# Performance work log

Measured on AMD Instinct MI355X. Metric: run time of the kernel, lower is better.

The kernel has to match this reference:

```python
import jax, jax.numpy as jnp
import numpy as np

EPS = 1e-6
MAX_ACOSH_ARG = 1e6
MAX_DIST = 50.0
TINY = 1e-15
B, T, D = 2, 512, 512
H, N = 8, 32
A = N + 1
TAU = 1.0


def mink(x, y):
    # Lorentzian inner product over last (ambient) dim
    return -x[..., 0] * y[..., 0] + jnp.sum(x[..., 1:] * y[..., 1:], axis=-1)


def project_to_hyperboloid(x):
    xx = mink(x, x)
    scale = jnp.sqrt(jnp.maximum(jnp.abs(xx), TINY))[..., None]
    x = x / scale
    return jnp.concatenate([jnp.abs(x[..., :1]), x[..., 1:]], axis=-1)


def exp_map(p, v):
    vn = jnp.sqrt(jnp.maximum(mink(v, v), TINY))[..., None]
    y = jnp.cosh(vn) * p + (jnp.sinh(vn) / jnp.maximum(vn, TINY)) * v
    return project_to_hyperboloid(y)


def log_map(p, y):
    alpha = jnp.clip(-mink(p, y), 1.0 + EPS, MAX_ACOSH_ARG)
    dist = jnp.arccosh(alpha)[..., None]
    u = y + alpha[..., None] * p
    un = jnp.sqrt(jnp.maximum(mink(u, u), TINY))[..., None]
    return dist / jnp.maximum(un, TINY) * u


def _lift(x, W, b):
    # Linear lift -> (B,H,T,N), append time-like 0, expmap at origin
    u = (jnp.einsum('btd,dk->btk', x, W) + b).reshape(B, T, H, N).transpose(0, 2, 1, 3)
    v = jnp.concatenate([jnp.zeros(u.shape[:-1] + (1,), u.dtype), u], axis=-1)  # (B,H,T,A)
    o = jnp.zeros((A,), u.dtype).at[0].set(1.0)
    return exp_map(jnp.broadcast_to(o, v.shape), v)


def setup_inputs() -> dict:
    key = jax.random.key(0)
    ks = jax.random.split(key, 5)
    x = jax.random.normal(ks[0], (B, T, D), jnp.float32)
    Wq = jax.random.normal(ks[1], (D, H * N), jnp.float32) * 0.02
    Wk = jax.random.normal(ks[2], (D, H * N), jnp.float32) * 0.02
    Wv = jax.random.normal(ks[3], (D, H * N), jnp.float32) * 0.02
    Wo = jax.random.normal(ks[4], (H * A, D), jnp.float32) * 0.02
    return {'x': x, 'Wq': Wq, 'bq': jnp.zeros((H * N,), jnp.float32),
            'Wk': Wk, 'bk': jnp.zeros((H * N,), jnp.float32),
            'Wv': Wv, 'bv': jnp.zeros((H * N,), jnp.float32),
            'Wo': Wo, 'bo': jnp.zeros((D,), jnp.float32)}


def reference(x, Wq, bq, Wk, bk, Wv, bv, Wo, bo):
    Q = _lift(x, Wq, bq)  # (B,H,T,A) on hyperboloid
    K = _lift(x, Wk, bk)
    V = _lift(x, Wv, bv)

    # pairwise hyperbolic distances: alpha = -<q,k>_L, d = acosh(alpha)
    alpha = jnp.clip(-mink(Q[:, :, :, None, :], K[:, :, None, :, :]), 1.0 + EPS, MAX_ACOSH_ARG)
    d = jnp.minimum(jnp.arccosh(alpha), MAX_DIST)  # (B,H,T,T)
    scores = -TAU * d * d
    attn = jax.nn.softmax(scores.astype(jnp.float32), axis=-1).astype(V.dtype)

    # one Karcher step around Q
    Y = Q
    logv = log_map(Y[:, :, :, None, :], V[:, :, None, :, :])  # (B,H,T,T,A)
    step = jnp.einsum('bhqk,bhqka->bhqa', attn, logv)
    step_norm = jnp.sqrt(jnp.maximum(mink(step, step), TINY))[..., None]
    step = step * (jnp.minimum(step_norm, 20.0) / (step_norm + 1e-9))
    Y = exp_map(Y, step)  # (B,H,T,A)

    # log-map at origin anchor, project back to d_model
    o = jnp.zeros((A,), Y.dtype).at[0].set(1.0)
    Yt = Y.transpose(0, 2, 1, 3)  # (B,T,H,A)
    p0 = jnp.broadcast_to(o, Yt.shape)
    Z_tan = log_map(p0, Yt).reshape(B, T, H * A)
    Z = jnp.einsum('btk,kd->btd', Z_tan, Wo) + bo
    return Z
```

## Files before the change

kernel.cpp:

```cpp
#include <hip/hip_runtime.h>
#include <math.h>

#define EPSF 1e-6f
#define MAX_ACOSH_ARGF 1e6f
#define MAX_DISTF 50.0f
#define TINYF 1e-15f

constexpr int QSZ  = 16 * 512 * 33;
constexpr int KTSZ = 16 * 9 * 512 * 4;
constexpr int ZTSZ = 1024 * 264;

__device__ __forceinline__ float facosh(float a) {
    return __logf(a + sqrtf((a - 1.0f) * (a + 1.0f)));
}
__device__ __forceinline__ float bcast(float x) {
    return __int_as_float(__builtin_amdgcn_readfirstlane(__float_as_int(x)));
}

__global__ __launch_bounds__(256) void qkv_kernel(
    const float* __restrict__ x,
    const float* __restrict__ Wq, const float* __restrict__ bq,
    const float* __restrict__ Wk, const float* __restrict__ bk,
    const float* __restrict__ Wv, const float* __restrict__ bv,
    float* __restrict__ Q, float* __restrict__ KT, float* __restrict__ VT)
{
    const int tid  = threadIdx.x;
    const int wiu  = __builtin_amdgcn_readfirstlane(tid >> 6);
    const int lane = tid & 63;
    const int gw   = blockIdx.x * 4 + wiu;
    const int ct   = gw % 6;
    const int mt   = gw / 6;
    const int m0   = mt * 8;
    const int tsel = ct >> 1;
    const int n0   = (ct & 1) * 128;
    const float* W    = (tsel == 0) ? Wq : (tsel == 1) ? Wk : Wv;
    const float* bias = (tsel == 0) ? bq : (tsel == 1) ? bk : bv;
    const int c0 = n0 + lane * 2;

    float acc[8][2];
    {
        const float b0 = bias[c0], b1 = bias[c0 + 1];
        #pragma unroll
        for (int r = 0; r < 8; ++r) { acc[r][0] = b0; acc[r][1] = b1; }
    }

    for (int kb = 0; kb < 512; kb += 8) {
        float xa[8][8];
        #pragma unroll
        for (int r = 0; r < 8; ++r) {
            const float4 t0 = *(const float4*)(x + (m0 + r) * 512 + kb);
            const float4 t1 = *(const float4*)(x + (m0 + r) * 512 + kb + 4);
            xa[r][0] = t0.x; xa[r][1] = t0.y; xa[r][2] = t0.z; xa[r][3] = t0.w;
            xa[r][4] = t1.x; xa[r][5] = t1.y; xa[r][6] = t1.z; xa[r][7] = t1.w;
        }
        #pragma unroll
        for (int k8 = 0; k8 < 8; ++k8) {
            const float2 bv2 = *(const float2*)(W + (kb + k8) * 256 + c0);
            #pragma unroll
            for (int r = 0; r < 8; ++r) {
                acc[r][0] = fmaf(xa[r][k8], bv2.x, acc[r][0]);
                acc[r][1] = fmaf(xa[r][k8], bv2.y, acc[r][1]);
            }
        }
    }

    const int cin = (lane & 15) * 2;
    const int h   = (n0 + lane * 2) >> 5;
    #pragma unroll
    for (int r = 0; r < 8; ++r) {
        const float e0 = acc[r][0], e1 = acc[r][1];
        float n2 = fmaf(e0, e0, e1 * e1);
        #pragma unroll
        for (int msk = 1; msk < 16; msk <<= 1) n2 += __shfl_xor(n2, msk, 64);
        n2 = fmaxf(n2, TINYF);
        const float vn = sqrtf(n2);
        const float ch = coshf(vn);
        const float sh = sinhf(vn) / fmaxf(vn, TINYF);
        const float xx = fmaf(sh * sh, n2, -ch * ch);
        const float scale = sqrtf(fmaxf(fabsf(xx), TINYF));
        const float fs = sh / scale;
        const int bt = m0 + r, b = bt >> 9, t = bt & 511;
        const int bh = b * 8 + h;
        if (tsel == 0) {
            float* qp = Q + (bh * 512 + t) * 33;
            qp[1 + cin] = fs * e0;
            qp[2 + cin] = fs * e1;
            if (cin == 0) qp[0] = fabsf(ch / scale);
        } else {
            float* P = ((tsel == 1) ? KT : VT) + bh * 18432;
            const int aa = 1 + cin, ab = 2 + cin;
            P[(aa >> 2) * 2048 + t * 4 + (aa & 3)] = fs * e0;
            P[(ab >> 2) * 2048 + t * 4 + (ab & 3)] = fs * e1;
            if (cin == 0) P[t * 4] = fabsf(ch / scale);
            if (cin == 30) {
                P[8 * 2048 + t * 4 + 1] = 0.0f;
                P[8 * 2048 + t * 4 + 2] = 0.0f;
                P[8 * 2048 + t * 4 + 3] = 0.0f;
            }
        }
    }
}

__global__ __launch_bounds__(256) void attn_kernel(
    const float* __restrict__ Q, const float* __restrict__ KT,
    const float* __restrict__ VT, float* __restrict__ ZT)
{
    __shared__ __align__(16) float4 sm4[2304 + 67];
    float* Qs = (float*)(sm4 + 2304);

    const int blk = blockIdx.x;
    const int bh  = blk >> 6;
    const int q0  = (blk & 63) * 8;
    const int tid = threadIdx.x;
    const int wiu = __builtin_amdgcn_readfirstlane(tid >> 6);
    const int k   = tid & 63;

    const float4* Ksrc = (const float4*)KT + bh * 4608;
    const float4* Vsrc = (const float4*)VT + bh * 4608;
    const float*  Qg   = Q + (bh * 512 + q0) * 33;

    for (int i = tid; i < 264; i += 256) Qs[i] = Qg[i];
    for (int idx = tid; idx < 1152; idx += 256) {
        const int mtx = idx >= 576 ? 1 : 0;
        const int rem = idx - mtx * 576;
        sm4[idx] = (mtx ? Vsrc : Ksrc)[(rem >> 6) * 512 + (rem & 63)];
    }
    __syncthreads();

    float qn0[36], qn1[36];
    {
        const int r0 = 2 * wiu, r1 = r0 + 1;
        #pragma unroll
        for (int a = 0; a < 36; ++a) {
            float v0 = (a < 33) ? Qs[r0 * 33 + a] : 0.0f;
            float v1 = (a < 33) ? Qs[r1 * 33 + a] : 0.0f;
            if (a >= 1) { v0 = -v0; v1 = -v1; }
            qn0[a] = bcast(v0); qn1[a] = bcast(v1);
        }
    }

    float mv0 = -3.0e38f, lv0 = 0.0f, sa0 = 0.0f;
    float mv1 = -3.0e38f, lv1 = 0.0f, sa1 = 0.0f;
    float ac0[33], ac1[33];
    #pragma unroll
    for (int a = 0; a < 33; ++a) { ac0[a] = 0.0f; ac1[a] = 0.0f; }

    for (int c = 0; c < 8; ++c) {
        if (c < 7) {
            const int cn = c + 1;
            const int bb = (cn & 1) * 1152;
            for (int idx = tid; idx < 1152; idx += 256) {
                const int mtx = idx >= 576 ? 1 : 0;
                const int rem = idx - mtx * 576;
                sm4[bb + idx] = (mtx ? Vsrc : Ksrc)[(rem >> 6) * 512 + cn * 64 + (rem & 63)];
            }
        }
        const float4* bK = sm4 + (c & 1) * 1152;
        const float4* bV = bK + 576;

        float kf[36];
        #pragma unroll
        for (int j = 0; j < 9; ++j) {
            const float4 t = bK[j * 64 + k];
            kf[4*j] = t.x; kf[4*j+1] = t.y; kf[4*j+2] = t.z; kf[4*j+3] = t.w;
        }
        float p00=0.f,p01=0.f,p02=0.f,p03=0.f, p10=0.f,p11=0.f,p12=0.f,p13=0.f;
        #pragma unroll
        for (int j = 0; j < 9; ++j) {
            p00 = fmaf(qn0[4*j],   kf[4*j],   p00);
            p01 = fmaf(qn0[4*j+1], kf[4*j+1], p01);
            p02 = fmaf(qn0[4*j+2], kf[4*j+2], p02);
            p03 = fmaf(qn0[4*j+3], kf[4*j+3], p03);
            p10 = fmaf(qn1[4*j],   kf[4*j],   p10);
            p11 = fmaf(qn1[4*j+1], kf[4*j+1], p11);
            p12 = fmaf(qn1[4*j+2], kf[4*j+2], p12);
            p13 = fmaf(qn1[4*j+3], kf[4*j+3], p13);
        }
        const float al10 = (p00 + p01) + (p02 + p03);
        const float al11 = (p10 + p11) + (p12 + p13);

        float vf[36];
        #pragma unroll
        for (int j = 0; j < 9; ++j) {
            const float4 t = bV[j * 64 + k];
            vf[4*j] = t.x; vf[4*j+1] = t.y; vf[4*j+2] = t.z; vf[4*j+3] = t.w;
        }
        float r00=0.f,r01=0.f,r02=0.f,r03=0.f, r10=0.f,r11=0.f,r12=0.f,r13=0.f;
        #pragma unroll
        for (int j = 0; j < 9; ++j) {
            r00 = fmaf(qn0[4*j],   vf[4*j],   r00);
            r01 = fmaf(qn0[4*j+1], vf[4*j+1], r01);
            r02 = fmaf(qn0[4*j+2], vf[4*j+2], r02);
            r03 = fmaf(qn0[4*j+3], vf[4*j+3], r03);
            r10 = fmaf(qn1[4*j],   vf[4*j],   r10);
            r11 = fmaf(qn1[4*j+1], vf[4*j+1], r11);
            r12 = fmaf(qn1[4*j+2], vf[4*j+2], r12);
            r13 = fmaf(qn1[4*j+3], vf[4*j+3], r13);
        }
        const float al20 = (r00 + r01) + (r02 + r03);
        const float al21 = (r10 + r11) + (r12 + r13);

        {
            const float a1c = fminf(fmaxf(al10, 1.0f + EPSF), MAX_ACOSH_ARGF);
            const float d1  = fminf(facosh(a1c), MAX_DISTF);
            const float sN  = -d1 * d1;
            const float a2c = fminf(fmaxf(al20, 1.0f + EPSF), MAX_ACOSH_ARGF);
            const float d2  = facosh(a2c);
            if (sN > mv0) {
                const float cr = __expf(mv0 - sN);
                lv0 *= cr; sa0 *= cr;
                #pragma unroll
                for (int a = 0; a < 33; ++a) ac0[a] *= cr;
                mv0 = sN;
            }
            const float e = __expf(sN - mv0);
            lv0 += e;
            const float w = e * d2;
            sa0 = fmaf(w, a2c, sa0);
            #pragma unroll
            for (int a = 0; a < 33; ++a) ac0[a] = fmaf(w, vf[a], ac0[a]);
        }
        {
            const float a1c = fminf(fmaxf(al11, 1.0f + EPSF), MAX_ACOSH_ARGF);
            const float d1  = fminf(facosh(a1c), MAX_DISTF);
            const float sN  = -d1 * d1;
            const float a2c = fminf(fmaxf(al21, 1.0f + EPSF), MAX_ACOSH_ARGF);
            const float d2  = facosh(a2c);
            if (sN > mv1) {
                const float cr = __expf(mv1 - sN);
                lv1 *= cr; sa1 *= cr;
                #pragma unroll
                for (int a = 0; a < 33; ++a) ac1[a] *= cr;
                mv1 = sN;
            }
            const float e = __expf(sN - mv1);
            lv1 += e;
            const float w = e * d2;
            sa1 = fmaf(w, a2c, sa1);
            #pragma unroll
            for (int a = 0; a < 33; ++a) ac1[a] = fmaf(w, vf[a], ac1[a]);
        }
        __syncthreads();
    }

    float M0 = mv0, M1 = mv1;
    #pragma unroll
    for (int msk = 1; msk < 64; msk <<= 1) {
        M0 = fmaxf(M0, __shfl_xor(M0, msk, 64));
        M1 = fmaxf(M1, __shfl_xor(M1, msk, 64));
    }
    const float cl0 = __expf(mv0 - M0), cl1 = __expf(mv1 - M1);
    float lw0 = lv0 * cl0, sw0 = sa0 * cl0;
    float lw1 = lv1 * cl1, sw1 = sa1 * cl1;
    #pragma unroll
    for (int msk = 1; msk < 64; msk <<= 1) {
        lw0 += __shfl_xor(lw0, msk, 64);
        sw0 += __shfl_xor(sw0, msk, 64);
        lw1 += __shfl_xor(lw1, msk, 64);
        sw1 += __shfl_xor(sw1, msk, 64);
    }
    #pragma unroll
    for (int a = 0; a < 33; ++a) {
        float v0 = ac0[a] * cl0, v1 = ac1[a] * cl1;
        #pragma unroll
        for (int msk = 1; msk < 64; msk <<= 1) {
            v0 += __shfl_xor(v0, msk, 64);
            v1 += __shfl_xor(v1, msk, 64);
        }
        ac0[a] = v0; ac1[a] = v1;
    }

    const int b = bh >> 3, h = bh & 7;
    const float un_c = sqrtf(TINYF);

    #pragma unroll
    for (int q = 0; q < 2; ++q) {
        float (&ac)[33] = q ? ac1 : ac0;
        float (&qn)[36] = q ? qn1 : qn0;
        const float lw = q ? lw1 : lw0;
        const float sw = q ? sw1 : sw0;
        const float inv_un = (1.0f / (q ? lw1 : lw0)) / un_c;
        ac[0] = fmaf(sw, qn[0], ac[0]) * inv_un;
        #pragma unroll
        for (int a = 1; a < 33; ++a) ac[a] = fmaf(-sw, qn[a], ac[a]) * inv_un;

        float mk = -ac[0] * ac[0];
        #pragma unroll
        for (int a = 1; a < 33; ++a) mk = fmaf(ac[a], ac[a], mk);
        const float snorm = sqrtf(fmaxf(mk, TINYF));
        const float fac   = fminf(snorm, 20.0f) / (snorm + 1e-9f);
        #pragma unroll
        for (int a = 0; a < 33; ++a) ac[a] *= fac;

        float mk2 = -ac[0] * ac[0];
        #pragma unroll
        for (int a = 1; a < 33; ++a) mk2 = fmaf(ac[a], ac[a], mk2);
        const float vn  = sqrtf(fmaxf(mk2, TINYF));
        const float ch  = coshf(vn);
        const float shr = sinhf(vn) / fmaxf(vn, TINYF);
        ac[0] = fmaf(ch, qn[0], shr * ac[0]);
        #pragma unroll
        for (int a = 1; a < 33; ++a) ac[a] = fmaf(-ch, qn[a], shr * ac[a]);

        float xx = -ac[0] * ac[0];
        #pragma unroll
        for (int a = 1; a < 33; ++a) xx = fmaf(ac[a], ac[a], xx);
        const float scale = sqrtf(fmaxf(fabsf(xx), TINYF));

        const float Y0  = fabsf(ac[0] / scale);
        const float al3 = fminf(fmaxf(Y0, 1.0f + EPSF), MAX_ACOSH_ARGF);
        const float d3  = acoshf(al3);
        const float f3  = d3 / un_c;

        if (k == q) {
            const int qi = q0 + 2 * wiu + q;
            float* zp = ZT + (b * 512 + qi) * 264 + h * 33;
            zp[0] = f3 * (Y0 + al3);
            const float fsc = f3 / scale;
            #pragma unroll
            for (int a = 1; a < 33; ++a) zp[a] = fsc * ac[a];
        }
        (void)lw;
    }
}

__global__ __launch_bounds__(256) void out_kernel(
    const float* __restrict__ ZT, const float* __restrict__ Wo,
    const float* __restrict__ bo, float* __restrict__ out)
{
    const int tid  = threadIdx.x;
    const int wiu  = __builtin_amdgcn_readfirstlane(tid >> 6);
    const int lane = tid & 63;
    const int gw   = blockIdx.x * 4 + wiu;
    const int mt   = gw >> 2;
    const int n0   = (gw & 3) * 128;
    const int m0   = mt * 4;
    const int c0   = n0 + lane * 2;

    float acc[4][2];
    {
        const float b0 = bo[c0], b1 = bo[c0 + 1];
        #pragma unroll
        for (int r = 0; r < 4; ++r) { acc[r][0] = b0; acc[r][1] = b1; }
    }

    for (int kb = 0; kb < 264; kb += 8) {
        float za[4][8];
        #pragma unroll
        for (int r = 0; r < 4; ++r) {
            const float4 t0 = *(const float4*)(ZT + (m0 + r) * 264 + kb);
            const float4 t1 = *(const float4*)(ZT + (m0 + r) * 264 + kb + 4);
            za[r][0] = t0.x; za[r][1] = t0.y; za[r][2] = t0.z; za[r][3] = t0.w;
            za[r][4] = t1.x; za[r][5] = t1.y; za[r][6] = t1.z; za[r][7] = t1.w;
        }
        #pragma unroll
        for (int k8 = 0; k8 < 8; ++k8) {
            const float2 bv2 = *(const float2*)(Wo + (kb + k8) * 512 + c0);
            #pragma unroll
            for (int r = 0; r < 4; ++r) {
                acc[r][0] = fmaf(za[r][k8], bv2.x, acc[r][0]);
                acc[r][1] = fmaf(za[r][k8], bv2.y, acc[r][1]);
            }
        }
    }
    #pragma unroll
    for (int r = 0; r < 4; ++r)
        *(float2*)(out + (m0 + r) * 512 + c0) = make_float2(acc[r][0], acc[r][1]);
}

extern "C" void kernel_launch(void* const* d_in, const int* in_sizes, int n_in,
                              void* d_out, int out_size, void* d_ws, size_t ws_size,
                              hipStream_t stream) {
    const float* x  = (const float*)d_in[0];
    const float* Wq = (const float*)d_in[1];
    const float* bq = (const float*)d_in[2];
    const float* Wk = (const float*)d_in[3];
    const float* bk = (const float*)d_in[4];
    const float* Wv = (const float*)d_in[5];
    const float* bv = (const float*)d_in[6];
    const float* Wo = (const float*)d_in[7];
    const float* bo = (const float*)d_in[8];
    float* out = (float*)d_out;
    float* ws  = (float*)d_ws;

    float* Q   = ws;
    float* KT  = ws + QSZ;
    float* VT  = ws + QSZ + KTSZ;
    float* ZTp = ws + QSZ + 2 * KTSZ;

    qkv_kernel<<<192, 256, 0, stream>>>(x, Wq, bq, Wk, bk, Wv, bv, Q, KT, VT);
    attn_kernel<<<1024, 256, 0, stream>>>(Q, KT, VT, ZTp);
    out_kernel<<<256, 256, 0, stream>>>(ZTp, Wo, bo, out);
}
```

Measured before the change: 212.3 us.

## Restructure attention to 16-lane key split per query and pipeline GEMM loads

```diff
diff --git a/kernel.cpp b/kernel.cpp
--- a/kernel.cpp
+++ b/kernel.cpp
@@ -6,68 +6,75 @@
 #define MAX_DISTF 50.0f
 #define TINYF 1e-15f
 
-constexpr int QSZ  = 16 * 512 * 33;
+typedef float f4v __attribute__((ext_vector_type(4)));
+typedef float f2v __attribute__((ext_vector_type(2)));
+
+constexpr int QPSZ = 16 * 512 * 36;
 constexpr int KTSZ = 16 * 9 * 512 * 4;
 constexpr int ZTSZ = 1024 * 264;
 
 __device__ __forceinline__ float facosh(float a) {
     return __logf(a + sqrtf((a - 1.0f) * (a + 1.0f)));
 }
-__device__ __forceinline__ float bcast(float x) {
-    return __int_as_float(__builtin_amdgcn_readfirstlane(__float_as_int(x)));
-}
-
-__global__ __launch_bounds__(256) void qkv_kernel(
+
+__global__ __launch_bounds__(64) void qkv_kernel(
     const float* __restrict__ x,
     const float* __restrict__ Wq, const float* __restrict__ bq,
     const float* __restrict__ Wk, const float* __restrict__ bk,
     const float* __restrict__ Wv, const float* __restrict__ bv,
-    float* __restrict__ Q, float* __restrict__ KT, float* __restrict__ VT)
+    float* __restrict__ Qp, float* __restrict__ KT, float* __restrict__ VT)
 {
-    const int tid  = threadIdx.x;
-    const int wiu  = __builtin_amdgcn_readfirstlane(tid >> 6);
-    const int lane = tid & 63;
-    const int gw   = blockIdx.x * 4 + wiu;
+    const int lane = threadIdx.x;
+    const int gw   = blockIdx.x;
     const int ct   = gw % 6;
     const int mt   = gw / 6;
-    const int m0   = mt * 8;
+    const int m0   = mt * 4;
     const int tsel = ct >> 1;
     const int n0   = (ct & 1) * 128;
     const float* W    = (tsel == 0) ? Wq : (tsel == 1) ? Wk : Wv;
     const float* bias = (tsel == 0) ? bq : (tsel == 1) ? bk : bv;
     const int c0 = n0 + lane * 2;
-
-    float acc[8][2];
+    const float* xb = x + m0 * 512;
+
+    float acc[4][2];
     {
         const float b0 = bias[c0], b1 = bias[c0 + 1];
         #pragma unroll
-        for (int r = 0; r < 8; ++r) { acc[r][0] = b0; acc[r][1] = b1; }
-    }
-
-    for (int kb = 0; kb < 512; kb += 8) {
-        float xa[8][8];
-        #pragma unroll
-        for (int r = 0; r < 8; ++r) {
-            const float4 t0 = *(const float4*)(x + (m0 + r) * 512 + kb);
-            const float4 t1 = *(const float4*)(x + (m0 + r) * 512 + kb + 4);
-            xa[r][0] = t0.x; xa[r][1] = t0.y; xa[r][2] = t0.z; xa[r][3] = t0.w;
-            xa[r][4] = t1.x; xa[r][5] = t1.y; xa[r][6] = t1.z; xa[r][7] = t1.w;
-        }
-        #pragma unroll
-        for (int k8 = 0; k8 < 8; ++k8) {
-            const float2 bv2 = *(const float2*)(W + (kb + k8) * 256 + c0);
-            #pragma unroll
-            for (int r = 0; r < 8; ++r) {
-                acc[r][0] = fmaf(xa[r][k8], bv2.x, acc[r][0]);
-                acc[r][1] = fmaf(xa[r][k8], bv2.y, acc[r][1]);
-            }
-        }
-    }
-
-    const int cin = (lane & 15) * 2;
-    const int h   = (n0 + lane * 2) >> 5;
-    #pragma unroll
-    for (int r = 0; r < 8; ++r) {
+        for (int r = 0; r < 4; ++r) { acc[r][0] = b0; acc[r][1] = b1; }
+    }
+
+    f4v aA[4][2], aB[4][2];
+    f2v bA[8], bB[8];
+
+#define LDA_Q(BUF, KB)                                            \
+    _Pragma("unroll") for (int r = 0; r < 4; ++r) {               \
+        BUF[r][0] = *(const f4v*)(xb + r * 512 + (KB));           \
+        BUF[r][1] = *(const f4v*)(xb + r * 512 + (KB) + 4);       \
+    }
+#define LDB_Q(BUF, KB)                                            \
+    _Pragma("unroll") for (int j = 0; j < 8; ++j)                 \
+        BUF[j] = *(const f2v*)(W + ((KB) + j) * 256 + c0);
+#define STEP_Q(AB, BB)                                            \
+    _Pragma("unroll") for (int j = 0; j < 8; ++j) {               \
+        _Pragma("unroll") for (int r = 0; r < 4; ++r) {           \
+            const float av = AB[r][j >> 2][j & 3];                \
+            acc[r][0] = fmaf(av, BB[j][0], acc[r][0]);            \
+            acc[r][1] = fmaf(av, BB[j][1], acc[r][1]);            \
+        }                                                         \
+    }
+
+    LDA_Q(aA, 0) LDB_Q(bA, 0)
+    for (int kb = 0; kb < 512; kb += 16) {
+        LDA_Q(aB, kb + 8) LDB_Q(bB, kb + 8)
+        STEP_Q(aA, bA)
+        if (kb + 16 < 512) { LDA_Q(aA, kb + 16) LDB_Q(bA, kb + 16) }
+        STEP_Q(aB, bB)
+    }
+
+    const int h   = c0 >> 5;
+    const int cin = c0 & 31;
+    #pragma unroll
+    for (int r = 0; r < 4; ++r) {
         const float e0 = acc[r][0], e1 = acc[r][1];
         float n2 = fmaf(e0, e0, e1 * e1);
         #pragma unroll
@@ -82,16 +89,17 @@
         const int bt = m0 + r, b = bt >> 9, t = bt & 511;
         const int bh = b * 8 + h;
         if (tsel == 0) {
-            float* qp = Q + (bh * 512 + t) * 33;
+            float* qp = Qp + (bh * 512 + t) * 36;
             qp[1 + cin] = fs * e0;
             qp[2 + cin] = fs * e1;
-            if (cin == 0) qp[0] = fabsf(ch / scale);
+            if (cin == 0)  qp[0] = fabsf(ch / scale);
+            if (cin == 30) { qp[33] = 0.0f; qp[34] = 0.0f; qp[35] = 0.0f; }
         } else {
             float* P = ((tsel == 1) ? KT : VT) + bh * 18432;
             const int aa = 1 + cin, ab = 2 + cin;
             P[(aa >> 2) * 2048 + t * 4 + (aa & 3)] = fs * e0;
             P[(ab >> 2) * 2048 + t * 4 + (ab & 3)] = fs * e1;
-            if (cin == 0) P[t * 4] = fabsf(ch / scale);
+            if (cin == 0)  P[t * 4] = fabsf(ch / scale);
             if (cin == 30) {
                 P[8 * 2048 + t * 4 + 1] = 0.0f;
                 P[8 * 2048 + t * 4 + 2] = 0.0f;
@@ -102,240 +110,163 @@
 }
 
 __global__ __launch_bounds__(256) void attn_kernel(
-    const float* __restrict__ Q, const float* __restrict__ KT,
+    const float* __restrict__ Qp, const float* __restrict__ KT,
     const float* __restrict__ VT, float* __restrict__ ZT)
 {
-    __shared__ __align__(16) float4 sm4[2304 + 67];
-    float* Qs = (float*)(sm4 + 2304);
-
-    const int blk = blockIdx.x;
-    const int bh  = blk >> 6;
-    const int q0  = (blk & 63) * 8;
-    const int tid = threadIdx.x;
-    const int wiu = __builtin_amdgcn_readfirstlane(tid >> 6);
-    const int k   = tid & 63;
-
-    const float4* Ksrc = (const float4*)KT + bh * 4608;
-    const float4* Vsrc = (const float4*)VT + bh * 4608;
-    const float*  Qg   = Q + (bh * 512 + q0) * 33;
-
-    for (int i = tid; i < 264; i += 256) Qs[i] = Qg[i];
-    for (int idx = tid; idx < 1152; idx += 256) {
-        const int mtx = idx >= 576 ? 1 : 0;
-        const int rem = idx - mtx * 576;
-        sm4[idx] = (mtx ? Vsrc : Ksrc)[(rem >> 6) * 512 + (rem & 63)];
-    }
-    __syncthreads();
-
-    float qn0[36], qn1[36];
+    const int tid  = threadIdx.x;
+    const int blk  = blockIdx.x;
+    const int bh   = blk >> 5;
+    const int q0   = (blk & 31) * 16;
+    const int wid  = tid >> 6;
+    const int lane = tid & 63;
+    const int g    = lane >> 4;
+    const int t    = lane & 15;
+    const int qi   = q0 + wid * 4 + g;
+
+    float qn[36];
     {
-        const int r0 = 2 * wiu, r1 = r0 + 1;
-        #pragma unroll
-        for (int a = 0; a < 36; ++a) {
-            float v0 = (a < 33) ? Qs[r0 * 33 + a] : 0.0f;
-            float v1 = (a < 33) ? Qs[r1 * 33 + a] : 0.0f;
-            if (a >= 1) { v0 = -v0; v1 = -v1; }
-            qn0[a] = bcast(v0); qn1[a] = bcast(v1);
-        }
-    }
-
-    float mv0 = -3.0e38f, lv0 = 0.0f, sa0 = 0.0f;
-    float mv1 = -3.0e38f, lv1 = 0.0f, sa1 = 0.0f;
-    float ac0[33], ac1[33];
-    #pragma unroll
-    for (int a = 0; a < 33; ++a) { ac0[a] = 0.0f; ac1[a] = 0.0f; }
-
-    for (int c = 0; c < 8; ++c) {
-        if (c < 7) {
-            const int cn = c + 1;
-            const int bb = (cn & 1) * 1152;
-            for (int idx = tid; idx < 1152; idx += 256) {
-                const int mtx = idx >= 576 ? 1 : 0;
-                const int rem = idx - mtx * 576;
-                sm4[bb + idx] = (mtx ? Vsrc : Ksrc)[(rem >> 6) * 512 + cn * 64 + (rem & 63)];
+        const float* qp = Qp + (bh * 512 + qi) * 36;
+        #pragma unroll
+        for (int j = 0; j < 9; ++j) {
+            const f4v v = *(const f4v*)(qp + 4 * j);
+            #pragma unroll
+            for (int i = 0; i < 4; ++i) {
+                const int a = 4 * j + i;
+                qn[a] = (a == 0) ? v[i] : -v[i];
             }
         }
-        const float4* bK = sm4 + (c & 1) * 1152;
-        const float4* bV = bK + 576;
-
-        float kf[36];
+    }
+
+    const f4v* K4 = (const f4v*)KT + bh * 4608;
+    const f4v* V4 = (const f4v*)VT + bh * 4608;
+
+    float m = -3.0e38f, l = 0.0f, s = 0.0f;
+    float ac[33];
+    #pragma unroll
+    for (int a = 0; a < 33; ++a) ac[a] = 0.0f;
+
+    for (int st = 0; st < 32; ++st) {
+        const int k = t + 16 * st;
+        f4v kr[9], vr[9];
+        #pragma unroll
+        for (int j = 0; j < 9; ++j) kr[j] = K4[j * 512 + k];
+        #pragma unroll
+        for (int j = 0; j < 9; ++j) vr[j] = V4[j * 512 + k];
+
+        float p0 = 0.f, p1 = 0.f, p2 = 0.f, p3 = 0.f;
         #pragma unroll
         for (int j = 0; j < 9; ++j) {
-            const float4 t = bK[j * 64 + k];
-            kf[4*j] = t.x; kf[4*j+1] = t.y; kf[4*j+2] = t.z; kf[4*j+3] = t.w;
-        }
-        float p00=0.f,p01=0.f,p02=0.f,p03=0.f, p10=0.f,p11=0.f,p12=0.f,p13=0.f;
+            p0 = fmaf(qn[4 * j],     kr[j][0], p0);
+            p1 = fmaf(qn[4 * j + 1], kr[j][1], p1);
+            p2 = fmaf(qn[4 * j + 2], kr[j][2], p2);
+            p3 = fmaf(qn[4 * j + 3], kr[j][3], p3);
+        }
+        const float a1 = (p0 + p1) + (p2 + p3);
+
+        float r0 = 0.f, r1 = 0.f, r2 = 0.f, r3 = 0.f;
         #pragma unroll
         for (int j = 0; j < 9; ++j) {
-            p00 = fmaf(qn0[4*j],   kf[4*j],   p00);
-            p01 = fmaf(qn0[4*j+1], kf[4*j+1], p01);
-            p02 = fmaf(qn0[4*j+2], kf[4*j+2], p02);
-            p03 = fmaf(qn0[4*j+3], kf[4*j+3], p03);
-            p10 = fmaf(qn1[4*j],   kf[4*j],   p10);
-            p11 = fmaf(qn1[4*j+1], kf[4*j+1], p11);
-            p12 = fmaf(qn1[4*j+2], kf[4*j+2], p12);
-            p13 = fmaf(qn1[4*j+3], kf[4*j+3], p13);
-        }
-        const float al10 = (p00 + p01) + (p02 + p03);
-        const float al11 = (p10 + p11) + (p12 + p13);
-
-        float vf[36];
-        #pragma unroll
-        for (int j = 0; j < 9; ++j) {
-            const float4 t = bV[j * 64 + k];
-            vf[4*j] = t.x; vf[4*j+1] = t.y; vf[4*j+2] = t.z; vf[4*j+3] = t.w;
-        }
-        float r00=0.f,r01=0.f,r02=0.f,r03=0.f, r10=0.f,r11=0.f,r12=0.f,r13=0.f;
-        #pragma unroll
-        for (int j = 0; j < 9; ++j) {
-            r00 = fmaf(qn0[4*j],   vf[4*j],   r00);
-            r01 = fmaf(qn0[4*j+1], vf[4*j+1], r01);
-            r02 = fmaf(qn0[4*j+2], vf[4*j+2], r02);
-            r03 = fmaf(qn0[4*j+3], vf[4*j+3], r03);
-            r10 = fmaf(qn1[4*j],   vf[4*j],   r10);
-            r11 = fmaf(qn1[4*j+1], vf[4*j+1], r11);
-            r12 = fmaf(qn1[4*j+2], vf[4*j+2], r12);
-            r13 = fmaf(qn1[4*j+3], vf[4*j+3], r13);
-        }
-        const float al20 = (r00 + r01) + (r02 + r03);
-        const float al21 = (r10 + r11) + (r12 + r13);
-
-        {
-            const float a1c = fminf(fmaxf(al10, 1.0f + EPSF), MAX_ACOSH_ARGF);
-            const float d1  = fminf(facosh(a1c), MAX_DISTF);
-            const float sN  = -d1 * d1;
-            const float a2c = fminf(fmaxf(al20, 1.0f + EPSF), MAX_ACOSH_ARGF);
-            const float d2  = facosh(a2c);
-            if (sN > mv0) {
-                const float cr = __expf(mv0 - sN);
-                lv0 *= cr; sa0 *= cr;
-                #pragma unroll
-                for (int a = 0; a < 33; ++a) ac0[a] *= cr;
-                mv0 = sN;
-            }
-            const float e = __expf(sN - mv0);
-            lv0 += e;
-            const float w = e * d2;
-            sa0 = fmaf(w, a2c, sa0);
+            r0 = fmaf(qn[4 * j],     vr[j][0], r0);
+            r1 = fmaf(qn[4 * j + 1], vr[j][1], r1);
+            r2 = fmaf(qn[4 * j + 2], vr[j][2], r2);
+            r3 = fmaf(qn[4 * j + 3], vr[j][3], r3);
+        }
+        const float a2 = (r0 + r1) + (r2 + r3);
+
+        const float a1c = fminf(fmaxf(a1, 1.0f + EPSF), MAX_ACOSH_ARGF);
+        const float d1  = fminf(facosh(a1c), MAX_DISTF);
+        const float sN  = -d1 * d1;
+        const float a2c = fminf(fmaxf(a2, 1.0f + EPSF), MAX_ACOSH_ARGF);
+        const float d2  = facosh(a2c);
+
+        if (sN > m) {
+            const float cr = __expf(m - sN);
+            l *= cr; s *= cr;
             #pragma unroll
-            for (int a = 0; a < 33; ++a) ac0[a] = fmaf(w, vf[a], ac0[a]);
-        }
-        {
-            const float a1c = fminf(fmaxf(al11, 1.0f + EPSF), MAX_ACOSH_ARGF);
-            const float d1  = fminf(facosh(a1c), MAX_DISTF);
-            const float sN  = -d1 * d1;
-            const float a2c = fminf(fmaxf(al21, 1.0f + EPSF), MAX_ACOSH_ARGF);
-            const float d2  = facosh(a2c);
-            if (sN > mv1) {
-                const float cr = __expf(mv1 - sN);
-                lv1 *= cr; sa1 *= cr;
-                #pragma unroll
-                for (int a = 0; a < 33; ++a) ac1[a] *= cr;
-                mv1 = sN;
-            }
-            const float e = __expf(sN - mv1);
-            lv1 += e;
-            const float w = e * d2;
-            sa1 = fmaf(w, a2c, sa1);
-            #pragma unroll
-            for (int a = 0; a < 33; ++a) ac1[a] = fmaf(w, vf[a], ac1[a]);
-        }
-        __syncthreads();
-    }
-
-    float M0 = mv0, M1 = mv1;
-    #pragma unroll
-    for (int msk = 1; msk < 64; msk <<= 1) {
-        M0 = fmaxf(M0, __shfl_xor(M0, msk, 64));
-        M1 = fmaxf(M1, __shfl_xor(M1, msk, 64));
-    }
-    const float cl0 = __expf(mv0 - M0), cl1 = __expf(mv1 - M1);
-    float lw0 = lv0 * cl0, sw0 = sa0 * cl0;
-    float lw1 = lv1 * cl1, sw1 = sa1 * cl1;
-    #pragma unroll
-    for (int msk = 1; msk < 64; msk <<= 1) {
-        lw0 += __shfl_xor(lw0, msk, 64);
-        sw0 += __shfl_xor(sw0, msk, 64);
-        lw1 += __shfl_xor(lw1, msk, 64);
-        sw1 += __shfl_xor(sw1, msk, 64);
+            for (int a = 0; a < 33; ++a) ac[a] *= cr;
+            m = sN;
+        }
+        const float e = __expf(sN - m);
+        l += e;
+        const float w = e * d2;
+        s = fmaf(w, a2c, s);
+        #pragma unroll
+        for (int a = 0; a < 33; ++a) ac[a] = fmaf(w, vr[a >> 2][a & 3], ac[a]);
+    }
+
+    float M = m;
+    #pragma unroll
+    for (int msk = 1; msk < 16; msk <<= 1) M = fmaxf(M, __shfl_xor(M, msk, 64));
+    const float cl = __expf(m - M);
+    float lw = l * cl, sw = s * cl;
+    #pragma unroll
+    for (int msk = 1; msk < 16; msk <<= 1) {
+        lw += __shfl_xor(lw, msk, 64);
+        sw += __shfl_xor(sw, msk, 64);
     }
     #pragma unroll
     for (int a = 0; a < 33; ++a) {
-        float v0 = ac0[a] * cl0, v1 = ac1[a] * cl1;
-        #pragma unroll
-        for (int msk = 1; msk < 64; msk <<= 1) {
-            v0 += __shfl_xor(v0, msk, 64);
-            v1 += __shfl_xor(v1, msk, 64);
-        }
-        ac0[a] = v0; ac1[a] = v1;
-    }
-
-    const int b = bh >> 3, h = bh & 7;
-    const float un_c = sqrtf(TINYF);
-
-    #pragma unroll
-    for (int q = 0; q < 2; ++q) {
-        float (&ac)[33] = q ? ac1 : ac0;
-        float (&qn)[36] = q ? qn1 : qn0;
-        const float lw = q ? lw1 : lw0;
-        const float sw = q ? sw1 : sw0;
-        const float inv_un = (1.0f / (q ? lw1 : lw0)) / un_c;
-        ac[0] = fmaf(sw, qn[0], ac[0]) * inv_un;
-        #pragma unroll
-        for (int a = 1; a < 33; ++a) ac[a] = fmaf(-sw, qn[a], ac[a]) * inv_un;
-
-        float mk = -ac[0] * ac[0];
-        #pragma unroll
-        for (int a = 1; a < 33; ++a) mk = fmaf(ac[a], ac[a], mk);
-        const float snorm = sqrtf(fmaxf(mk, TINYF));
-        const float fac   = fminf(snorm, 20.0f) / (snorm + 1e-9f);
-        #pragma unroll
-        for (int a = 0; a < 33; ++a) ac[a] *= fac;
-
-        float mk2 = -ac[0] * ac[0];
-        #pragma unroll
-        for (int a = 1; a < 33; ++a) mk2 = fmaf(ac[a], ac[a], mk2);
-        const float vn  = sqrtf(fmaxf(mk2, TINYF));
-        const float ch  = coshf(vn);
-        const float shr = sinhf(vn) / fmaxf(vn, TINYF);
-        ac[0] = fmaf(ch, qn[0], shr * ac[0]);
-        #pragma unroll
-        for (int a = 1; a < 33; ++a) ac[a] = fmaf(-ch, qn[a], shr * ac[a]);
-
-        float xx = -ac[0] * ac[0];
-        #pragma unroll
-        for (int a = 1; a < 33; ++a) xx = fmaf(ac[a], ac[a], xx);
-        const float scale = sqrtf(fmaxf(fabsf(xx), TINYF));
-
-        const float Y0  = fabsf(ac[0] / scale);
-        const float al3 = fminf(fmaxf(Y0, 1.0f + EPSF), MAX_ACOSH_ARGF);
-        const float d3  = acoshf(al3);
-        const float f3  = d3 / un_c;
-
-        if (k == q) {
-            const int qi = q0 + 2 * wiu + q;
-            float* zp = ZT + (b * 512 + qi) * 264 + h * 33;
-            zp[0] = f3 * (Y0 + al3);
-            const float fsc = f3 / scale;
-            #pragma unroll
-            for (int a = 1; a < 33; ++a) zp[a] = fsc * ac[a];
-        }
-        (void)lw;
-    }
-}
-
-__global__ __launch_bounds__(256) void out_kernel(
+        float v = ac[a] * cl;
+        #pragma unroll
+        for (int msk = 1; msk < 16; msk <<= 1) v += __shfl_xor(v, msk, 64);
+        ac[a] = v;
+    }
+
+    const float un_c  = sqrtf(TINYF);
+    const float inv_un = (1.0f / lw) / un_c;
+    ac[0] = fmaf(sw, qn[0], ac[0]) * inv_un;
+    #pragma unroll
+    for (int a = 1; a < 33; ++a) ac[a] = fmaf(-sw, qn[a], ac[a]) * inv_un;
+
+    float mk = -ac[0] * ac[0];
+    #pragma unroll
+    for (int a = 1; a < 33; ++a) mk = fmaf(ac[a], ac[a], mk);
+    const float snorm = sqrtf(fmaxf(mk, TINYF));
+    const float fac   = fminf(snorm, 20.0f) / (snorm + 1e-9f);
+    #pragma unroll
+    for (int a = 0; a < 33; ++a) ac[a] *= fac;
+
+    float mk2 = -ac[0] * ac[0];
+    #pragma unroll
+    for (int a = 1; a < 33; ++a) mk2 = fmaf(ac[a], ac[a], mk2);
+    const float vn  = sqrtf(fmaxf(mk2, TINYF));
+    const float ch  = coshf(vn);
+    const float shr = sinhf(vn) / fmaxf(vn, TINYF);
+    ac[0] = fmaf(ch, qn[0], shr * ac[0]);
+    #pragma unroll
+    for (int a = 1; a < 33; ++a) ac[a] = fmaf(-ch, qn[a], shr * ac[a]);
+
+    float xx = -ac[0] * ac[0];
+    #pragma unroll
+    for (int a = 1; a < 33; ++a) xx = fmaf(ac[a], ac[a], xx);
+    const float scale = sqrtf(fmaxf(fabsf(xx), TINYF));
+
+    const float Y0  = fabsf(ac[0] / scale);
+    const float al3 = fminf(fmaxf(Y0, 1.0f + EPSF), MAX_ACOSH_ARGF);
+    const float d3  = acoshf(al3);
+    const float f3  = d3 / un_c;
+
+    if (t == 0) {
+        const int b = bh >> 3, h = bh & 7;
+        float* zp = ZT + (b * 512 + qi) * 264 + h * 33;
+        zp[0] = f3 * (Y0 + al3);
+        const float fsc = f3 / scale;
+        #pragma unroll
+        for (int a = 1; a < 33; ++a) zp[a] = fsc * ac[a];
+    }
+}
+
+__global__ __launch_bounds__(64) void out_kernel(
     const float* __restrict__ ZT, const float* __restrict__ Wo,
     const float* __restrict__ bo, float* __restrict__ out)
 {
-    const int tid  = threadIdx.x;
-    const int wiu  = __builtin_amdgcn_readfirstlane(tid >> 6);
-    const int lane = tid & 63;
-    const int gw   = blockIdx.x * 4 + wiu;
+    const int lane = threadIdx.x;
+    const int gw   = blockIdx.x;
     const int mt   = gw >> 2;
+    const int m0   = mt * 4;
     const int n0   = (gw & 3) * 128;
-    const int m0   = mt * 4;
     const int c0   = n0 + lane * 2;
+    const float* zb = ZT + m0 * 264;
 
     float acc[4][2];
     {
@@ -344,28 +275,38 @@
         for (int r = 0; r < 4; ++r) { acc[r][0] = b0; acc[r][1] = b1; }
     }
 
-    for (int kb = 0; kb < 264; kb += 8) {
-        float za[4][8];
-        #pragma unroll
-        for (int r = 0; r < 4; ++r) {
-            const float4 t0 = *(const float4*)(ZT + (m0 + r) * 264 + kb);
-            const float4 t1 = *(const float4*)(ZT + (m0 + r) * 264 + kb + 4);
-            za[r][0] = t0.x; za[r][1] = t0.y; za[r][2] = t0.z; za[r][3] = t0.w;
-            za[r][4] = t1.x; za[r][5] = t1.y; za[r][6] = t1.z; za[r][7] = t1.w;
-        }
-        #pragma unroll
-        for (int k8 = 0; k8 < 8; ++k8) {
-            const float2 bv2 = *(const float2*)(Wo + (kb + k8) * 512 + c0);
-            #pragma unroll
-            for (int r = 0; r < 4; ++r) {
-                acc[r][0] = fmaf(za[r][k8], bv2.x, acc[r][0]);
-                acc[r][1] = fmaf(za[r][k8], bv2.y, acc[r][1]);
-            }
-        }
-    }
+    f4v aA[4][2], aB[4][2];
+    f2v bA[8], bB[8];
+
+#define LDA_O(BUF, KB)                                            \
+    _Pragma("unroll") for (int r = 0; r < 4; ++r) {               \
+        BUF[r][0] = *(const f4v*)(zb + r * 264 + (KB));           \
+        BUF[r][1] = *(const f4v*)(zb + r * 264 + (KB) + 4);       \
+    }
+#define LDB_O(BUF, KB)                                            \
+    _Pragma("unroll") for (int j = 0; j < 8; ++j)                 \
+        BUF[j] = *(const f2v*)(Wo + ((KB) + j) * 512 + c0);
+#define STEP_O(AB, BB)                                            \
+    _Pragma("unroll") for (int j = 0; j < 8; ++j) {               \
+        _Pragma("unroll") for (int r = 0; r < 4; ++r) {           \
+            const float av = AB[r][j >> 2][j & 3];                \
+            acc[r][0] = fmaf(av, BB[j][0], acc[r][0]);            \
+            acc[r][1] = fmaf(av, BB[j][1], acc[r][1]);            \
+        }                                                         \
+    }
+
+    LDA_O(aA, 0) LDB_O(bA, 0)
+    for (int kb = 0; kb < 256; kb += 16) {
+        LDA_O(aB, kb + 8) LDB_O(bB, kb + 8)
+        STEP_O(aA, bA)
+        LDA_O(aA, kb + 16) LDB_O(bA, kb + 16)
+        STEP_O(aB, bB)
+    }
+    STEP_O(aA, bA)
+
     #pragma unroll
     for (int r = 0; r < 4; ++r)
-        *(float2*)(out + (m0 + r) * 512 + c0) = make_float2(acc[r][0], acc[r][1]);
+        *(f2v*)(out + (m0 + r) * 512 + c0) = f2v{acc[r][0], acc[r][1]};
 }
 
 extern "C" void kernel_launch(void* const* d_in, const int* in_sizes, int n_in,
@@ -383,12 +324,12 @@
     float* out = (float*)d_out;
     float* ws  = (float*)d_ws;
 
-    float* Q   = ws;
-    float* KT  = ws + QSZ;
-    float* VT  = ws + QSZ + KTSZ;
-    float* ZTp = ws + QSZ + 2 * KTSZ;
-
-    qkv_kernel<<<192, 256, 0, stream>>>(x, Wq, bq, Wk, bk, Wv, bv, Q, KT, VT);
-    attn_kernel<<<1024, 256, 0, stream>>>(Q, KT, VT, ZTp);
-    out_kernel<<<256, 256, 0, stream>>>(ZTp, Wo, bo, out);
-}
+    float* Qp  = ws;
+    float* KT  = ws + QPSZ;
+    float* VT  = ws + QPSZ + KTSZ;
+    float* ZTp = ws + QPSZ + 2 * KTSZ;
+
+    qkv_kernel<<<1536, 64, 0, stream>>>(x, Wq, bq, Wk, bk, Wv, bv, Qp, KT, VT);
+    attn_kernel<<<512, 256, 0, stream>>>(Qp, KT, VT, ZTp);
+    out_kernel<<<1024, 64, 0, stream>>>(ZTp, Wo, bo, out);
+}
```

After: 171.7 us. 1.24x faster.
